# Performance work log

Hardware: AMD Instinct MI355X
Metric: run time of the kernel (lower is better)

The kernel has to match this reference:

```python
import jax, jax.numpy as jnp
import numpy as np

B, N, A = 8, 8192, 10   # batch, points, attributes (xyz + normal + 4 extra)
G, M = 512, 32          # num_group, group_size
EPS = 1e-5


def setup_inputs() -> dict:
    key = jax.random.key(0)
    ks = jax.random.split(key, 16)
    w = lambda k, s: jax.random.normal(k, s, jnp.float32) * 0.02
    inp = {"xyz": jax.random.normal(ks[0], (B, N, A), jnp.float32)}
    # Light_T_Net params (conv1 6->64, conv2 64->512, fc 512->36)
    inp["tn_w1"], inp["tn_b1"] = w(ks[1], (64, 6)), jnp.zeros(64, jnp.float32)
    inp["tn_g1"], inp["tn_be1"] = jnp.ones(64, jnp.float32), jnp.zeros(64, jnp.float32)
    inp["tn_w2"], inp["tn_b2"] = w(ks[2], (512, 64)), jnp.zeros(512, jnp.float32)
    inp["tn_g2"], inp["tn_be2"] = jnp.ones(512, jnp.float32), jnp.zeros(512, jnp.float32)
    inp["tn_fw"], inp["tn_fb"] = w(ks[3], (36, 512)), jnp.zeros(36, jnp.float32)
    # Light_PointNet_Encoder convs: A->128->256->512->1024
    for i, (co, ci) in enumerate([(128, A), (256, 128), (512, 256), (1024, 512)], 1):
        inp[f"w{i}"], inp[f"b{i}"] = w(ks[3 + i], (co, ci)), jnp.zeros(co, jnp.float32)
        inp[f"g{i}"], inp[f"be{i}"] = jnp.ones(co, jnp.float32), jnp.zeros(co, jnp.float32)
    return inp


def _bn(x, g, b):
    # training-mode BatchNorm1d: stats over (batch, length) for [BG, n, C]
    m = x.mean((0, 1))
    v = x.var((0, 1))
    return (x - m) * jax.lax.rsqrt(v + EPS) * g + b


def _fps(xyz, npoint):
    # sequential farthest-point sampling (deterministic start index 0)
    coords = xyz[:, :, :3]
    b, n, _ = xyz.shape

    def step(carry, _):
        dist, far = carry
        cen = jnp.take_along_axis(xyz, far[:, None, None], axis=1)  # [B,1,A]
        d = jnp.sum((coords - cen[:, :, :3]) ** 2, -1)              # [B,N]
        dist = jnp.minimum(dist, d)
        return (dist, jnp.argmax(dist, -1)), (far, cen[:, 0, :])

    dist0 = jnp.full((b, n), 1e10, xyz.dtype)
    far0 = jnp.zeros((b,), jnp.int32)
    _, (idx, attrs) = jax.lax.scan(step, (dist0, far0), None, length=npoint)
    return idx.T, attrs.transpose(1, 0, 2)  # [B,G], [B,G,A]


def _forward(xyz, tn_w1, tn_b1, tn_g1, tn_be1, tn_w2, tn_b2, tn_g2, tn_be2,
             tn_fw, tn_fb, w1, b1, g1, be1, w2, b2, g2, be2,
             w3, b3, g3, be3, w4, b4, g4, be4):
    b = xyz.shape[0]
    # ---- Group_for_all_attribute ----
    _, cen = _fps(xyz, G)                                           # [B,G,A]
    # cdist over full attribute dim; squared distance gives identical topk order
    d2 = (jnp.sum(cen ** 2, -1)[:, :, None] + jnp.sum(xyz ** 2, -1)[:, None, :]
          - 2.0 * jnp.einsum('bga,bna->bgn', cen, xyz))             # [B,G,N]
    idx = jax.lax.top_k(-d2, M)[1]                                  # [B,G,M] smallest dists
    nb = xyz[jnp.arange(b)[:, None, None], idx]                     # [B,G,M,A]
    nb = jnp.concatenate([nb[..., :3] - cen[:, :, None, :3], nb[..., 3:]], -1)
    # ---- Light_PointNet_Encoder ----
    pg = nb.reshape(b * G, M, A)
    x6 = pg[:, :, :6]
    # Light_T_Net
    h = jax.nn.relu(_bn(x6 @ tn_w1.T + tn_b1, tn_g1, tn_be1))
    h = jax.nn.relu(_bn(h @ tn_w2.T + tn_b2, tn_g2, tn_be2))
    t = (h.max(1) @ tn_fw.T + tn_fb + jnp.eye(6, dtype=xyz.dtype).reshape(36)).reshape(-1, 6, 6)
    pg = jnp.concatenate([jnp.einsum('bnc,bcd->bnd', x6, t), pg[:, :, 6:]], -1)
    # 1x1 conv stack (= per-point linear) with training-mode BN
    h = jax.nn.relu(_bn(pg @ w1.T + b1, g1, be1))
    h = jax.nn.relu(_bn(h @ w2.T + b2, g2, be2))
    h = jax.nn.relu(_bn(h @ w3.T + b3, g3, be3))
    h = _bn(h @ w4.T + b4, g4, be4)
    return h.max(1).reshape(b, G, -1)                               # [B,G,1024]


def reference(xyz, tn_w1, tn_b1, tn_g1, tn_be1, tn_w2, tn_b2, tn_g2, tn_be2,
              tn_fw, tn_fb, w1, b1, g1, be1, w2, b2, g2, be2,
              w3, b3, g3, be3, w4, b4, g4, be4):
    return _forward(xyz, tn_w1, tn_b1, tn_g1, tn_be1, tn_w2, tn_b2, tn_g2, tn_be2,
                    tn_fw, tn_fb, w1, b1, g1, be1, w2, b2, g2, be2,
                    w3, b3, g3, be3, w4, b4, g4, be4)
```

## Files before the change

### kernel.cpp

```cpp
#include <hip/hip_runtime.h>
#include <hip/hip_bf16.h>

static constexpr int B_  = 8;
static constexpr int N_  = 8192;
static constexpr int A_  = 10;
static constexpr int G_  = 512;
static constexpr int M_  = 32;
static constexpr int S_TOT = B_ * G_ * M_;
static constexpr float EPS_ = 1e-5f;
static constexpr float FMAXV = 3.402823466e+38f;

__device__ __forceinline__ float b2f(__hip_bfloat16 h) { return __bfloat162float(h); }
__device__ __forceinline__ unsigned short f2bs(float f) {
    __hip_bfloat16 h = __float2bfloat16(f);
    return *reinterpret_cast<unsigned short*>(&h);
}

typedef __bf16 bf16x8 __attribute__((ext_vector_type(8)));
typedef float  f32x4  __attribute__((ext_vector_type(4)));

__device__ __forceinline__ unsigned long long shfl_down_u64(unsigned long long v, int off) {
    unsigned lo = (unsigned)v, hi = (unsigned)(v >> 32);
    lo = __shfl_down(lo, off);
    hi = __shfl_down(hi, off);
    return ((unsigned long long)hi << 32) | lo;
}

static constexpr size_t CO_XYZ  = 0;
static constexpr size_t CO_TNW1 = 655360, CO_TNB1 = 655744, CO_TNG1 = 655808, CO_TNBE1 = 655872;
static constexpr size_t CO_TNW2 = 655936, CO_TNB2 = 688704, CO_TNG2 = 689216, CO_TNBE2 = 689728;
static constexpr size_t CO_TNFW = 690240, CO_TNFB = 708672;
static constexpr size_t CO_W1 = 708708, CO_B1 = 709988, CO_G1 = 710116, CO_BE1 = 710244;
static constexpr size_t CO_W2 = 710372, CO_B2 = 743140, CO_G2 = 743396, CO_BE2 = 743652;
static constexpr size_t CO_W3 = 743908, CO_B3 = 874980, CO_G3 = 875492, CO_BE3 = 876004;
static constexpr size_t CO_W4 = 876516, CO_B4 = 1400804, CO_G4 = 1401828, CO_BE4 = 1402852;
static constexpr size_t CO_TOT = 1403876;

static constexpr size_t WB_TNW2 = 0;
static constexpr size_t WB_W2   = 32768;
static constexpr size_t WB_W3   = 65536;
static constexpr size_t WB_W4   = 196608;
static constexpr size_t WB_TOT  = 720896;

#define MB_ (1024ull * 1024ull)
static constexpr size_t OFF_CANON = 0;
static constexpr size_t OFF_CEN   = 6 * MB_;
static constexpr size_t OFF_XSQ   = 6 * MB_ + 256 * 1024;
static constexpr size_t OFF_STATS = 6 * MB_ + 512 * 1024;
static constexpr size_t OFF_COEFF = 6 * MB_ + 576 * 1024;
static constexpr size_t OFF_DUMMY = 6 * MB_ + 640 * 1024;
static constexpr size_t OFF_TMAT  = 6 * MB_ + 768 * 1024;
static constexpr size_t OFF_WBF16 = 8 * MB_;
static constexpr size_t OFF_PG    = 10 * MB_;
static constexpr size_t OFF_TZ1   = 16 * MB_;
static constexpr size_t OFF_TPMAX = 32 * MB_;
static constexpr size_t OFF_TPMIN = 40 * MB_;
static constexpr size_t OFF_Z1    = 16 * MB_;
static constexpr size_t OFF_MM4X  = 16 * MB_;
static constexpr size_t OFF_MM4N  = 32 * MB_;
static constexpr size_t OFF_Z2    = 48 * MB_;
static constexpr size_t OFF_Z3    = 112 * MB_;
static constexpr size_t NEED_A = 240 * MB_;
static constexpr int NCHUNK_ = 8;
static constexpr int CSAMP_  = S_TOT / NCHUNK_;

static constexpr int STF_T1 = 0;
static constexpr int STF_T2 = 128;
static constexpr int STF_M1 = 1152;
static constexpr int STF_M2 = 1408;
static constexpr int STF_M3 = 1920;
static constexpr int STF_M4 = 2944;

struct Ptrs { const void* p[27]; };

__global__ __launch_bounds__(256)
void zero_kernel(float* __restrict__ p, int n)
{
    for (int i = threadIdx.x; i < n; i += 256) p[i] = 0.f;
}

__global__ __launch_bounds__(256)
void convert_kernel(Ptrs ptrs, float* __restrict__ canon)
{
    const size_t gid = (size_t)blockIdx.x * 256 + threadIdx.x;
    if (gid >= CO_TOT) return;
    constexpr size_t offs[28] = {0, 655360, 655744, 655808, 655872, 655936,
        688704, 689216, 689728, 690240, 708672, 708708, 709988, 710116, 710244,
        710372, 743140, 743396, 743652, 743908, 874980, 875492, 876004, 876516,
        1400804, 1401828, 1402852, 1403876};
    int j = 0;
    while (j < 26 && gid >= offs[j + 1]) ++j;
    const size_t loc = gid - offs[j];
    const bool fp32m = (((const unsigned short*)ptrs.p[3])[0] == 0);
    float v;
    if (fp32m) v = ((const float*)ptrs.p[j])[loc];
    else       v = b2f(((const __hip_bfloat16*)ptrs.p[j])[loc]);
    canon[gid] = v;
}

__global__ __launch_bounds__(256)
void wconv_kernel(const float* __restrict__ canon, __hip_bfloat16* __restrict__ wb)
{
    const size_t gid = (size_t)blockIdx.x * 256 + threadIdx.x;
    if (gid >= WB_TOT) return;
    constexpr size_t offs[5] = {0, 32768, 65536, 196608, 720896};
    constexpr size_t co[4]   = {CO_TNW2, CO_W2, CO_W3, CO_W4};
    int j = 0;
    while (j < 3 && gid >= offs[j + 1]) ++j;
    wb[gid] = __float2bfloat16(canon[co[j] + (gid - offs[j])]);
}

__global__ __launch_bounds__(256)
void fps_kernel(const float* __restrict__ xyz, float* __restrict__ cen)
{
    __shared__ float lx[N_], ly[N_], lz[N_];
    __shared__ unsigned long long red[2][4];
    __shared__ int fidx[G_];

    const int t = threadIdx.x;
    const int b = blockIdx.x;
    const float* xb = xyz + (size_t)b * N_ * A_;

    float px[32], py[32], pz[32], dist[32];
#pragma unroll
    for (int j = 0; j < 32; ++j) {
        const int i = j * 256 + t;
        px[j] = xb[(size_t)i * A_ + 0];
        py[j] = xb[(size_t)i * A_ + 1];
        pz[j] = xb[(size_t)i * A_ + 2];
        lx[i] = px[j]; ly[i] = py[j]; lz[i] = pz[j];
        dist[j] = 1e10f;
    }
    __syncthreads();

    int far = 0;
    for (int it = 0; it < G_; ++it) {
        if (t == 0) fidx[it] = far;
        const float cx = lx[far], cy = ly[far], cz = lz[far];

        float bv = -1.f; int bi = 0;
#pragma unroll
        for (int j = 0; j < 32; ++j) {
            const float dx = px[j] - cx, dy = py[j] - cy, dz = pz[j] - cz;
            const float d = dx * dx + dy * dy + dz * dz;
            const float nd = fminf(dist[j], d);
            dist[j] = nd;
            if (nd > bv) { bv = nd; bi = j * 256 + t; }
        }
        unsigned long long best =
            ((unsigned long long)__float_as_uint(bv) << 32) | (unsigned)~(unsigned)bi;
#pragma unroll
        for (int off = 32; off; off >>= 1) {
            const unsigned long long o = shfl_down_u64(best, off);
            best = (o > best) ? o : best;
        }
        const int p = it & 1;
        if ((t & 63) == 0) red[p][t >> 6] = best;
        __syncthreads();
        unsigned long long m = red[p][0];
#pragma unroll
        for (int w = 1; w < 4; ++w) {
            const unsigned long long o = red[p][w];
            m = (o > m) ? o : m;
        }
        far = (int)(~(unsigned)m) & (N_ - 1);
    }
    __syncthreads();
    for (int e = t; e < G_ * A_; e += 256) {
        const int it = e / A_;
        const int a  = e - it * A_;
        cen[((size_t)b * G_ + it) * A_ + a] = xb[(size_t)fidx[it] * A_ + a];
    }
}

__global__ __launch_bounds__(256)
void xsq_kernel(const float* __restrict__ xyz, float* __restrict__ xsq)
{
    const int i = blockIdx.x * 256 + threadIdx.x;
    float s = 0.f;
#pragma unroll
    for (int a = 0; a < A_; ++a) { const float v = xyz[(size_t)i * A_ + a]; s += v * v; }
    xsq[i] = s;
}

__global__ __launch_bounds__(256)
void knn_kernel(const float* __restrict__ xyz, const float* __restrict__ cen,
                const float* __restrict__ xsq, float* __restrict__ pg)
{
    __shared__ float d2[N_];
    __shared__ float ca[A_];
    __shared__ float csqs;
    __shared__ float redV[4];
    __shared__ int   redI[4];
    __shared__ int   win[M_];
    __shared__ int   curwin;

    const int t  = threadIdx.x;
    const int bg = blockIdx.x;
    const int b  = bg >> 9;
    const float* xb  = xyz + (size_t)b * N_ * A_;
    const float* xsb = xsq + (size_t)b * N_;

    if (t < A_) ca[t] = cen[(size_t)bg * A_ + t];
    __syncthreads();
    if (t == 0) {
        float s = 0.f;
        for (int a = 0; a < A_; ++a) s += ca[a] * ca[a];
        csqs = s;
    }
    __syncthreads();
    const float csq = csqs;

    for (int j = 0; j < 32; ++j) {
        const int i = j * 256 + t;
        float dot = 0.f;
#pragma unroll
        for (int a = 0; a < A_; ++a) dot += xb[(size_t)i * A_ + a] * ca[a];
        d2[i] = (csq + xsb[i]) - 2.f * dot;
    }
    __syncthreads();

    float bv = FMAXV; int bi = 0;
    for (int j = 0; j < 32; ++j) {
        const int i = j * 256 + t;
        const float v = d2[i];
        if (v < bv) { bv = v; bi = i; }
    }

    for (int it = 0; it < M_; ++it) {
        float rv = bv; int ri = bi;
#pragma unroll
        for (int off = 32; off; off >>= 1) {
            const float ov = __shfl_down(rv, off);
            const int   oi = __shfl_down(ri, off);
            if (ov < rv || (ov == rv && oi < ri)) { rv = ov; ri = oi; }
        }
        if ((t & 63) == 0) { redV[t >> 6] = rv; redI[t >> 6] = ri; }
        __syncthreads();
        if (t == 0) {
            float v = redV[0]; int wi = redI[0];
            for (int w = 1; w < 4; ++w)
                if (redV[w] < v || (redV[w] == v && redI[w] < wi)) { v = redV[w]; wi = redI[w]; }
            win[it] = wi; curwin = wi; d2[wi] = FMAXV;
        }
        __syncthreads();
        const int wi = curwin;
        if ((wi & 255) == t) {
            bv = FMAXV; bi = 0;
            for (int j = 0; j < 32; ++j) {
                const int i = j * 256 + t;
                const float v = d2[i];
                if (v < bv) { bv = v; bi = i; }
            }
        }
    }
    __syncthreads();
    if (t < M_) {
        const int i = win[t];
        for (int a = 0; a < A_; ++a) {
            float v = xb[(size_t)i * A_ + a];
            if (a < 3) v -= ca[a];
            pg[((size_t)bg * M_ + t) * A_ + a] = v;
        }
    }
}

template<int K, int C>
__global__ __launch_bounds__(256)
void mlp_small_kernel(const float* __restrict__ pgx,
                      const float* __restrict__ W,
                      const float* __restrict__ Bv,
                      __hip_bfloat16* __restrict__ Zout,
                      float* __restrict__ stats)
{
    __shared__ float w[C * K];
    __shared__ float bb[C];
    __shared__ float lstat[C][2];
    const int t = threadIdx.x;
    for (int i = t; i < C * K; i += 256) w[i] = W[i];
    for (int i = t; i < C; i += 256) bb[i] = Bv[i];
    for (int i = t; i < 2 * C; i += 256) ((float*)lstat)[i] = 0.f;
    __syncthreads();

    const size_t s = (size_t)blockIdx.x * 256 + t;
    float x[K];
#pragma unroll
    for (int k = 0; k < K; ++k) x[k] = pgx[s * A_ + k];

    ushort4 u;
    for (int c = 0; c < C; ++c) {
        float z = bb[c];
#pragma unroll
        for (int k = 0; k < K; ++k) z += w[c * K + k] * x[k];
        const unsigned short zs = f2bs(z);
        const int cm = c & 3;
        if (cm == 0) u.x = zs; else if (cm == 1) u.y = zs; else if (cm == 2) u.z = zs;
        else { u.w = zs; *reinterpret_cast<ushort4*>(Zout + s * C + (c - 3)) = u; }

        float sv = z, sq = z * z;
#pragma unroll
        for (int off = 32; off; off >>= 1) {
            sv += __shfl_down(sv, off);
            sq += __shfl_down(sq, off);
        }
        if ((t & 63) == 0) { atomicAdd(&lstat[c][0], sv); atomicAdd(&lstat[c][1], sq); }
    }
    __syncthreads();
    for (int c = t; c < C; c += 256) {
        atomicAdd(&stats[c],     lstat[c][0]);
        atomicAdd(&stats[C + c], lstat[c][1]);
    }
}

__global__ __launch_bounds__(256)
void finalize_kernel(const float* __restrict__ stats, const float* __restrict__ g,
                     const float* __restrict__ be, float* __restrict__ coeff, int C)
{
    for (int c = threadIdx.x; c < C; c += 256) {
        const float mean = stats[c] * (1.f / (float)S_TOT);
        const float var  = stats[C + c] * (1.f / (float)S_TOT) - mean * mean;
        const float sc = g[c] * rsqrtf(fmaxf(var, 0.f) + EPS_);
        coeff[c]     = sc;
        coeff[C + c] = be[c] - mean * sc;
    }
}

template<int K, int N, bool POOL>
__global__ __launch_bounds__(256)
void gemm_mfma_kernel(const __hip_bfloat16* __restrict__ Zin,
                      const float* __restrict__ coeff,
                      const __hip_bfloat16* __restrict__ Wb,
                      const float* __restrict__ Bv,
                      __hip_bfloat16* __restrict__ Zout,
                      float* __restrict__ maxbuf,
                      float* __restrict__ minbuf,
                      float* __restrict__ stats)
{
    constexpr int PITCH = 72;
    __shared__ __hip_bfloat16 As[128 * PITCH];
    __shared__ __hip_bfloat16 Bs[128 * PITCH];
    __shared__ float csc[K];
    __shared__ float csh[K];
    __shared__ float lstat[256];

    const int t    = threadIdx.x;
    const int lane = t & 63;
    const int wave = t >> 6;
    const int wm   = wave >> 1;
    const int wn   = wave & 1;
    const int ln   = lane & 15;
    const int quad = lane >> 4;
    const int c0   = blockIdx.x * 128;
    const int s0   = blockIdx.y * 128;

    for (int i = t; i < K; i += 256) { csc[i] = coeff[i]; csh[i] = coeff[K + i]; }
    lstat[t] = 0.f;

    f32x4 acc[4][4];
#pragma unroll
    for (int ni = 0; ni < 4; ++ni) {
        const float bj = Bv[c0 + wn * 64 + ni * 16 + ln];
#pragma unroll
        for (int mi = 0; mi < 4; ++mi) acc[mi][ni] = (f32x4){bj, bj, bj, bj};
    }

    for (int kt = 0; kt < K; kt += 64) {
        __syncthreads();
#pragma unroll
        for (int p = 0; p < 4; ++p) {
            const int id = p * 256 + t;
            const int r  = id >> 3;
            const int sg = id & 7;
            const float4 raw = *reinterpret_cast<const float4*>(
                Zin + (size_t)(s0 + r) * K + kt + sg * 8);
            const __hip_bfloat162* p2 = reinterpret_cast<const __hip_bfloat162*>(&raw);
            unsigned short tmp[8] __attribute__((aligned(16)));
#pragma unroll
            for (int j = 0; j < 4; ++j) {
                const int k0 = kt + sg * 8 + 2 * j;
                const float x0 = fmaxf(b2f(p2[j].x) * csc[k0]     + csh[k0],     0.f);
                const float x1 = fmaxf(b2f(p2[j].y) * csc[k0 + 1] + csh[k0 + 1], 0.f);
                tmp[2 * j]     = f2bs(x0);
                tmp[2 * j + 1] = f2bs(x1);
            }
            *reinterpret_cast<float4*>(&As[r * PITCH + sg * 8]) =
                *reinterpret_cast<const float4*>(tmp);
            *reinterpret_cast<float4*>(&Bs[r * PITCH + sg * 8]) =
                *reinterpret_cast<const float4*>(Wb + (size_t)(c0 + r) * K + kt + sg * 8);
        }
        __syncthreads();

        bf16x8 af[4][2], bf_[4][2];
#pragma unroll
        for (int mi = 0; mi < 4; ++mi)
#pragma unroll
            for (int kk = 0; kk < 2; ++kk)
                af[mi][kk] = *reinterpret_cast<const bf16x8*>(
                    &As[(wm * 64 + mi * 16 + ln) * PITCH + quad * 8 + kk * 32]);
#pragma unroll
        for (int ni = 0; ni < 4; ++ni)
#pragma unroll
            for (int kk = 0; kk < 2; ++kk)
                bf_[ni][kk] = *reinterpret_cast<const bf16x8*>(
                    &Bs[(wn * 64 + ni * 16 + ln) * PITCH + quad * 8 + kk * 32]);
#pragma unroll
        for (int kk = 0; kk < 2; ++kk)
#pragma unroll
            for (int mi = 0; mi < 4; ++mi)
#pragma unroll
                for (int ni = 0; ni < 4; ++ni)
                    acc[mi][ni] = __builtin_amdgcn_mfma_f32_16x16x32_bf16(
                        af[mi][kk], bf_[ni][kk], acc[mi][ni], 0, 0, 0);
    }

#pragma unroll
    for (int ni = 0; ni < 4; ++ni) {
        float sv = 0.f, sq = 0.f;
#pragma unroll
        for (int mi = 0; mi < 4; ++mi)
#pragma unroll
            for (int r = 0; r < 4; ++r) {
                const float v = acc[mi][ni][r];
                sv += v; sq += v * v;
            }
        sv += __shfl_xor(sv, 16); sq += __shfl_xor(sq, 16);
        sv += __shfl_xor(sv, 32); sq += __shfl_xor(sq, 32);
        if (quad == 0) {
            const int col = wn * 64 + ni * 16 + ln;
            atomicAdd(&lstat[col], sv);
            atomicAdd(&lstat[128 + col], sq);
        }
    }
    __syncthreads();
    if (t < 128) {
        atomicAdd(&stats[c0 + t],     lstat[t]);
        atomicAdd(&stats[N + c0 + t], lstat[128 + t]);
    }

    if constexpr (POOL) {
#pragma unroll
        for (int ni = 0; ni < 4; ++ni) {
            float mx0 = -FMAXV, mn0 = FMAXV, mx1 = -FMAXV, mn1 = FMAXV;
#pragma unroll
            for (int mi = 0; mi < 2; ++mi)
#pragma unroll
                for (int r = 0; r < 4; ++r) {
                    const float v = acc[mi][ni][r];
                    mx0 = fmaxf(mx0, v); mn0 = fminf(mn0, v);
                }
#pragma unroll
            for (int mi = 2; mi < 4; ++mi)
#pragma unroll
                for (int r = 0; r < 4; ++r) {
                    const float v = acc[mi][ni][r];
                    mx1 = fmaxf(mx1, v); mn1 = fminf(mn1, v);
                }
            mx0 = fmaxf(mx0, __shfl_xor(mx0, 16)); mn0 = fminf(mn0, __shfl_xor(mn0, 16));
            mx0 = fmaxf(mx0, __shfl_xor(mx0, 32)); mn0 = fminf(mn0, __shfl_xor(mn0, 32));
            mx1 = fmaxf(mx1, __shfl_xor(mx1, 16)); mn1 = fminf(mn1, __shfl_xor(mn1, 16));
            mx1 = fmaxf(mx1, __shfl_xor(mx1, 32)); mn1 = fminf(mn1, __shfl_xor(mn1, 32));
            if (quad == 0) {
                const int col = c0 + wn * 64 + ni * 16 + ln;
                const int g   = (s0 >> 5) + wm * 2;
                maxbuf[(size_t)g * N + col]       = mx0;
                minbuf[(size_t)g * N + col]       = mn0;
                maxbuf[(size_t)(g + 1) * N + col] = mx1;
                minbuf[(size_t)(g + 1) * N + col] = mn1;
            }
        }
    } else {
#pragma unroll
        for (int mi = 0; mi < 4; ++mi)
#pragma unroll
            for (int r = 0; r < 4; ++r) {
                const size_t row = (size_t)(s0 + wm * 64 + mi * 16 + quad * 4 + r);
#pragma unroll
                for (int ni = 0; ni < 4; ++ni) {
                    const int col = c0 + wn * 64 + ni * 16 + ln;
                    Zout[row * N + col] = __float2bfloat16(acc[mi][ni][r]);
                }
            }
    }
}

__global__ __launch_bounds__(64)
void tnet_fc_kernel(const float* __restrict__ maxbuf, const float* __restrict__ minbuf,
                    const float* __restrict__ coeff, const float* __restrict__ FW,
                    const float* __restrict__ FB, float* __restrict__ tmat)
{
    __shared__ float h[512];
    const int bg = blockIdx.x;
    const int t  = threadIdx.x;
    for (int i = t; i < 512; i += 64) {
        const float sc = coeff[i], sh = coeff[512 + i];
        const float v = (sc >= 0.f) ? maxbuf[(size_t)bg * 512 + i] : minbuf[(size_t)bg * 512 + i];
        h[i] = fmaxf(sc * v + sh, 0.f);
    }
    __syncthreads();
    if (t < 36) {
        float acc = FB[t] + ((t % 7 == 0) ? 1.f : 0.f);
        for (int k = 0; k < 512; ++k) acc += FW[t * 512 + k] * h[k];
        tmat[(size_t)bg * 36 + t] = acc;
    }
}

__global__ __launch_bounds__(256)
void transform_kernel(float* __restrict__ pg, const float* __restrict__ tmat)
{
    const size_t s = (size_t)blockIdx.x * 256 + threadIdx.x;
    const int bg = (int)(s >> 5);
    float x[6];
#pragma unroll
    for (int c = 0; c < 6; ++c) x[c] = pg[s * A_ + c];
    const float* tm = tmat + (size_t)bg * 36;
#pragma unroll
    for (int d = 0; d < 6; ++d) {
        float o = 0.f;
#pragma unroll
        for (int c = 0; c < 6; ++c) o += x[c] * tm[c * 6 + d];
        pg[s * A_ + d] = o;
    }
}

__global__ __launch_bounds__(256)
void output_kernel(const float* __restrict__ maxbuf, const float* __restrict__ minbuf,
                   const float* __restrict__ coeff, const unsigned short* __restrict__ probe,
                   void* __restrict__ out)
{
    const size_t e = (size_t)blockIdx.x * 256 + threadIdx.x;
    const int c = (int)(e & 1023);
    const float sc = coeff[c], sh = coeff[1024 + c];
    const float v = (sc >= 0.f) ? maxbuf[e] : minbuf[e];
    const float r = sc * v + sh;
    if (probe[0] == 0) ((float*)out)[e] = r;
    else ((__hip_bfloat16*)out)[e] = __float2bfloat16(r);
}

extern "C" void kernel_launch(void* const* d_in, const int* in_sizes, int n_in,
                              void* d_out, int out_size, void* d_ws, size_t ws_size,
                              hipStream_t stream)
{
    char* ws = (char*)d_ws;
    float*          canon = (float*)(ws + OFF_CANON);
    float*          cen   = (float*)(ws + OFF_CEN);
    float*          xsq   = (float*)(ws + OFF_XSQ);
    float*          stats = (float*)(ws + OFF_STATS);
    float*          coeff = (float*)(ws + OFF_COEFF);
    float*          dummy = (float*)(ws + OFF_DUMMY);
    float*          tmat  = (float*)(ws + OFF_TMAT);
    __hip_bfloat16* wbf   = (__hip_bfloat16*)(ws + OFF_WBF16);
    float*          tpmax = (float*)(ws + OFF_TPMAX);
    float*          tpmin = (float*)(ws + OFF_TPMIN);
    float*          pg    = (float*)(ws + OFF_PG);
    __hip_bfloat16* tz1   = (__hip_bfloat16*)(ws + OFF_TZ1);
    __hip_bfloat16* z1    = (__hip_bfloat16*)(ws + OFF_Z1);
    __hip_bfloat16* z2    = (__hip_bfloat16*)(ws + OFF_Z2);
    __hip_bfloat16* z3    = (__hip_bfloat16*)(ws + OFF_Z3);
    float*          mmax4 = (float*)(ws + OFF_MM4X);
    float*          mmin4 = (float*)(ws + OFF_MM4N);

    Ptrs ptrs;
    for (int i = 0; i < 27; ++i) ptrs.p[i] = d_in[i];

    const float* cxyz = canon + CO_XYZ;

    zero_kernel<<<1, 256, 0, stream>>>(stats, 5120);
    convert_kernel<<<(int)((CO_TOT + 255) / 256), 256, 0, stream>>>(ptrs, canon);
    wconv_kernel<<<(int)((WB_TOT + 255) / 256), 256, 0, stream>>>(canon, wbf);

    fps_kernel<<<B_, 256, 0, stream>>>(cxyz, cen);
    xsq_kernel<<<(B_ * N_) / 256, 256, 0, stream>>>(cxyz, xsq);
    knn_kernel<<<B_ * G_, 256, 0, stream>>>(cxyz, cen, xsq, pg);

    mlp_small_kernel<6, 64><<<S_TOT / 256, 256, 0, stream>>>(
        pg, canon + CO_TNW1, canon + CO_TNB1, tz1, stats + STF_T1);
    finalize_kernel<<<1, 256, 0, stream>>>(stats + STF_T1, canon + CO_TNG1, canon + CO_TNBE1,
                                           coeff + STF_T1, 64);
    gemm_mfma_kernel<64, 512, true><<<dim3(4, S_TOT / 128), 256, 0, stream>>>(
        tz1, coeff + STF_T1, wbf + WB_TNW2, canon + CO_TNB2, nullptr, tpmax, tpmin, stats + STF_T2);
    finalize_kernel<<<1, 256, 0, stream>>>(stats + STF_T2, canon + CO_TNG2, canon + CO_TNBE2,
                                           coeff + STF_T2, 512);
    tnet_fc_kernel<<<B_ * G_, 64, 0, stream>>>(tpmax, tpmin, coeff + STF_T2,
                                               canon + CO_TNFW, canon + CO_TNFB, tmat);
    transform_kernel<<<S_TOT / 256, 256, 0, stream>>>(pg, tmat);

    mlp_small_kernel<10, 128><<<S_TOT / 256, 256, 0, stream>>>(
        pg, canon + CO_W1, canon + CO_B1, z1, stats + STF_M1);
    finalize_kernel<<<1, 256, 0, stream>>>(stats + STF_M1, canon + CO_G1, canon + CO_BE1,
                                           coeff + STF_M1, 128);
    gemm_mfma_kernel<128, 256, false><<<dim3(2, S_TOT / 128), 256, 0, stream>>>(
        z1, coeff + STF_M1, wbf + WB_W2, canon + CO_B2, z2, nullptr, nullptr, stats + STF_M2);
    finalize_kernel<<<1, 256, 0, stream>>>(stats + STF_M2, canon + CO_G2, canon + CO_BE2,
                                           coeff + STF_M2, 256);

    if (ws_size >= NEED_A) {
        gemm_mfma_kernel<256, 512, false><<<dim3(4, S_TOT / 128), 256, 0, stream>>>(
            z2, coeff + STF_M2, wbf + WB_W3, canon + CO_B3, z3, nullptr, nullptr, stats + STF_M3);
        finalize_kernel<<<1, 256, 0, stream>>>(stats + STF_M3, canon + CO_G3, canon + CO_BE3,
                                               coeff + STF_M3, 512);
        gemm_mfma_kernel<512, 1024, true><<<dim3(8, S_TOT / 128), 256, 0, stream>>>(
            z3, coeff + STF_M3, wbf + WB_W4, canon + CO_B4, nullptr, mmax4, mmin4, stats + STF_M4);
    } else {
        for (int c = 0; c < NCHUNK_; ++c) {
            gemm_mfma_kernel<256, 512, false><<<dim3(4, CSAMP_ / 128), 256, 0, stream>>>(
                z2 + (size_t)c * CSAMP_ * 256, coeff + STF_M2, wbf + WB_W3, canon + CO_B3,
                z3, nullptr, nullptr, stats + STF_M3);
        }
        finalize_kernel<<<1, 256, 0, stream>>>(stats + STF_M3, canon + CO_G3, canon + CO_BE3,
                                               coeff + STF_M3, 512);
        for (int c = 0; c < NCHUNK_; ++c) {
            gemm_mfma_kernel<256, 512, false><<<dim3(4, CSAMP_ / 128), 256, 0, stream>>>(
                z2 + (size_t)c * CSAMP_ * 256, coeff + STF_M2, wbf + WB_W3, canon + CO_B3,
                z3, nullptr, nullptr, dummy);
            gemm_mfma_kernel<512, 1024, true><<<dim3(8, CSAMP_ / 128), 256, 0, stream>>>(
                z3, coeff + STF_M3, wbf + WB_W4, canon + CO_B4, nullptr,
                mmax4 + (size_t)(c * CSAMP_ / 32) * 1024,
                mmin4 + (size_t)(c * CSAMP_ / 32) * 1024, stats + STF_M4);
        }
    }
    finalize_kernel<<<1, 256, 0, stream>>>(stats + STF_M4, canon + CO_G4, canon + CO_BE4,
                                           coeff + STF_M4, 1024);

    output_kernel<<<(B_ * G_ * 1024) / 256, 256, 0, stream>>>(
        mmax4, mmin4, coeff + STF_M4, (const unsigned short*)d_in[3], d_out);
}
```

Before: 1.527 ms.

## Keep KNN distances in registers and use packed 64-bit key reduction

```diff
diff --git a/kernel.cpp b/kernel.cpp
--- a/kernel.cpp
+++ b/kernel.cpp
@@ -24,6 +24,11 @@
     lo = __shfl_down(lo, off);
     hi = __shfl_down(hi, off);
     return ((unsigned long long)hi << 32) | lo;
+}
+
+__device__ __forceinline__ unsigned fkey(float f) {
+    unsigned u = __float_as_uint(f);
+    return u ^ ((unsigned)((int)u >> 31) | 0x80000000u);
 }
 
 static constexpr size_t CO_XYZ  = 0;
@@ -74,15 +79,10 @@
 struct Ptrs { const void* p[27]; };
 
 __global__ __launch_bounds__(256)
-void zero_kernel(float* __restrict__ p, int n)
-{
-    for (int i = threadIdx.x; i < n; i += 256) p[i] = 0.f;
-}
-
-__global__ __launch_bounds__(256)
-void convert_kernel(Ptrs ptrs, float* __restrict__ canon)
+void convert_kernel(Ptrs ptrs, float* __restrict__ canon, float* __restrict__ stats)
 {
     const size_t gid = (size_t)blockIdx.x * 256 + threadIdx.x;
+    if (gid < 5120) stats[gid] = 0.f;
     if (gid >= CO_TOT) return;
     constexpr size_t offs[28] = {0, 655360, 655744, 655808, 655872, 655936,
         688704, 689216, 689728, 690240, 708672, 708708, 709988, 710116, 710244,
@@ -187,13 +187,9 @@
 void knn_kernel(const float* __restrict__ xyz, const float* __restrict__ cen,
                 const float* __restrict__ xsq, float* __restrict__ pg)
 {
-    __shared__ float d2[N_];
     __shared__ float ca[A_];
-    __shared__ float csqs;
-    __shared__ float redV[4];
-    __shared__ int   redI[4];
-    __shared__ int   win[M_];
-    __shared__ int   curwin;
+    __shared__ unsigned long long red[2][4];
+    __shared__ int win[M_];
 
     const int t  = threadIdx.x;
     const int bg = blockIdx.x;
@@ -203,54 +199,51 @@
 
     if (t < A_) ca[t] = cen[(size_t)bg * A_ + t];
     __syncthreads();
-    if (t == 0) {
-        float s = 0.f;
-        for (int a = 0; a < A_; ++a) s += ca[a] * ca[a];
-        csqs = s;
-    }
-    __syncthreads();
-    const float csq = csqs;
-
+    float csq = 0.f;
+#pragma unroll
+    for (int a = 0; a < A_; ++a) csq += ca[a] * ca[a];
+
+    float d2r[32];
+    float bv = FMAXV; int bi = 0;
+#pragma unroll
     for (int j = 0; j < 32; ++j) {
         const int i = j * 256 + t;
         float dot = 0.f;
 #pragma unroll
         for (int a = 0; a < A_; ++a) dot += xb[(size_t)i * A_ + a] * ca[a];
-        d2[i] = (csq + xsb[i]) - 2.f * dot;
-    }
-    __syncthreads();
-
-    float bv = FMAXV; int bi = 0;
-    for (int j = 0; j < 32; ++j) {
-        const int i = j * 256 + t;
-        const float v = d2[i];
+        const float v = (csq + xsb[i]) - 2.f * dot;
+        d2r[j] = v;
         if (v < bv) { bv = v; bi = i; }
     }
 
     for (int it = 0; it < M_; ++it) {
-        float rv = bv; int ri = bi;
+        unsigned long long key =
+            ((unsigned long long)fkey(bv) << 32) | (unsigned)bi;
 #pragma unroll
         for (int off = 32; off; off >>= 1) {
-            const float ov = __shfl_down(rv, off);
-            const int   oi = __shfl_down(ri, off);
-            if (ov < rv || (ov == rv && oi < ri)) { rv = ov; ri = oi; }
-        }
-        if ((t & 63) == 0) { redV[t >> 6] = rv; redI[t >> 6] = ri; }
+            const unsigned long long o = shfl_down_u64(key, off);
+            key = (o < key) ? o : key;
+        }
+        const int p = it & 1;
+        if ((t & 63) == 0) red[p][t >> 6] = key;
         __syncthreads();
-        if (t == 0) {
-            float v = redV[0]; int wi = redI[0];
-            for (int w = 1; w < 4; ++w)
-                if (redV[w] < v || (redV[w] == v && redI[w] < wi)) { v = redV[w]; wi = redI[w]; }
-            win[it] = wi; curwin = wi; d2[wi] = FMAXV;
-        }
-        __syncthreads();
-        const int wi = curwin;
-        if ((wi & 255) == t) {
+        unsigned long long m = red[p][0];
+#pragma unroll
+        for (int w = 1; w < 4; ++w) {
+            const unsigned long long o = red[p][w];
+            m = (o < m) ? o : m;
+        }
+        const int wi = (int)((unsigned)m) & (N_ - 1);
+        if (t == (wi & 255)) {
+            win[it] = wi;
+            const int wj = wi >> 8;
+#pragma unroll
+            for (int j = 0; j < 32; ++j) if (j == wj) d2r[j] = FMAXV;
             bv = FMAXV; bi = 0;
+#pragma unroll
             for (int j = 0; j < 32; ++j) {
-                const int i = j * 256 + t;
-                const float v = d2[i];
-                if (v < bv) { bv = v; bi = i; }
+                const float v = d2r[j];
+                if (v < bv) { bv = v; bi = j * 256 + t; }
             }
         }
     }
@@ -564,8 +557,7 @@
 
     const float* cxyz = canon + CO_XYZ;
 
-    zero_kernel<<<1, 256, 0, stream>>>(stats, 5120);
-    convert_kernel<<<(int)((CO_TOT + 255) / 256), 256, 0, stream>>>(ptrs, canon);
+    convert_kernel<<<(int)((CO_TOT + 255) / 256), 256, 0, stream>>>(ptrs, canon, stats);
     wconv_kernel<<<(int)((WB_TOT + 255) / 256), 256, 0, stream>>>(canon, wbf);
 
     fps_kernel<<<B_, 256, 0, stream>>>(cxyz, cen);
```

Result: no change. 1.512 ms (-1.0%).
